# Kernel tuning notes

Hardware: AMD Instinct MI355X
Metric: run time of the kernel (lower is better)

## Reference

```python
import jax, jax.numpy as jnp
import numpy as np


def setup_inputs() -> dict:
    key = jax.random.key(0)
    k1, k2, k3 = jax.random.split(key, 3)
    B, U, D0, D1 = 256, 512, 512, 1024
    x = jax.random.normal(k1, (B, D0), dtype=jnp.float32)
    y = jax.random.normal(k2, (B, D1), dtype=jnp.float32)
    # Glorot-uniform-ish scale for the bilinear weight
    limit = np.sqrt(6.0 / (D0 + D1)).astype(np.float32)
    w = jax.random.uniform(k3, (U, D0, D1), dtype=jnp.float32, minval=-limit, maxval=limit)
    b = jnp.zeros((U,), dtype=jnp.float32)
    return {"x": x, "y": y, "w": w, "b": b}


def reference(x, y, w, b):
    # out[b,u] = sum_{i,j} x[b,i] * w[u,i,j] * y[b,j] + b[u]
    # Two chained GEMMs instead of materializing (B,U,D0,D1):
    xw = jnp.einsum('bi,uij->buj', x, w)   # (B, U, D1)
    out = jnp.einsum('buj,bj->bu', xw, y) + b  # (B, U)
    return out
```

## Files before the change

### kernel.cpp

```cpp
#include <hip/hip_runtime.h>
#include <hip/hip_bf16.h>

typedef float f32x4 __attribute__((ext_vector_type(4)));
typedef short s16x8 __attribute__((ext_vector_type(8)));

#define NB   256
#define NU   512
#define ND0  512
#define ND1  1024
#define WROW (ND0 * ND1)

__device__ __forceinline__ unsigned int f2bf_pk(float a, float b) {
  __hip_bfloat16 ha = __float2bfloat16(a);
  __hip_bfloat16 hb = __float2bfloat16(b);
  unsigned short ua, ub;
  __builtin_memcpy(&ua, &ha, 2);
  __builtin_memcpy(&ub, &hb, 2);
  return (unsigned int)ua | ((unsigned int)ub << 16);
}

__device__ __forceinline__ void block_sync_lds() {
  asm volatile("s_waitcnt lgkmcnt(0)" ::: "memory");
  __builtin_amdgcn_s_barrier();
}

__global__ __launch_bounds__(256) void init_out(const float* __restrict__ bias,
                                                float* __restrict__ out) {
  int idx = blockIdx.x * 256 + threadIdx.x;
  out[idx] = bias[idx & (NU - 1)];
}

__global__ __launch_bounds__(512, 4) void bilinear_kern(
    const float* __restrict__ x, const float* __restrict__ y,
    const float* __restrict__ w, float* __restrict__ out) {
  __shared__ char Alds[32768];
  __shared__ char Wlds[16384];

  const int t    = threadIdx.x;
  const int lane = t & 63;
  const int l15  = lane & 15;
  const int lk   = lane >> 4;
  const int wid  = t >> 6;
  const int wm   = wid >> 2;
  const int wn   = wid & 3;

  const int nt    = blockIdx.x & 3;
  const int ic    = blockIdx.x >> 2;
  const int ucol0 = nt * 128 + wn * 32;

  f32x4 acc[8][2];
#pragma unroll
  for (int mf = 0; mf < 8; ++mf)
#pragma unroll
    for (int nf = 0; nf < 2; ++nf)
#pragma unroll
      for (int r = 0; r < 4; ++r) acc[mf][nf][r] = 0.0f;

  const int ar   = t >> 4;
  const int aswz = (ar & 7) << 4;
  const int awr  = ar * 128 + ((l15 * 8) ^ aswz);
  const float* yb = y + (size_t)ar * ND1 + l15 * 4;

  const int wrb = wid * 16 + lk;
  const float* wq = w + (size_t)(nt * 128 + wrb) * WROW + l15 * 4;

  const int afswz = (l15 & 7) << 4;

  f32x4 wv[4], wvn[4];
  {
    const float* p0 = wq + (size_t)(ic * 4) * ND1;
#pragma unroll
    for (int q = 0; q < 4; ++q)
      wv[q] = __builtin_nontemporal_load((const f32x4*)(p0 + (size_t)q * 4 * WROW));
  }
  float xv[8];
#pragma unroll
  for (int p = 0; p < 8; ++p)
    xv[p] = x[(size_t)(ar + 32 * p) * ND0 + ic * 4];

  for (int it = 0; it < 64; ++it) {
    const int j0 = (it & 15) * 64;

    block_sync_lds();

#pragma unroll
    for (int g = 0; g < 2; ++g) {
      f32x4 v[4];
#pragma unroll
      for (int pp = 0; pp < 4; ++pp)
        v[pp] = *(const f32x4*)(yb + (size_t)(g * 4 + pp) * 32 * ND1 + j0);
#pragma unroll
      for (int pp = 0; pp < 4; ++pp) {
        const int p = g * 4 + pp;
        unsigned long long pk =
            (unsigned long long)f2bf_pk(xv[p] * v[pp][0], xv[p] * v[pp][1]) |
            ((unsigned long long)f2bf_pk(xv[p] * v[pp][2], xv[p] * v[pp][3]) << 32);
        *(unsigned long long*)(Alds + awr + p * 4096) = pk;
      }
    }

#pragma unroll
    for (int q = 0; q < 4; ++q) {
      const int row  = wrb + 4 * q;
      const int byte = row * 128 + ((l15 * 8) ^ ((row & 7) << 4));
      unsigned long long pk =
          (unsigned long long)f2bf_pk(wv[q][0], wv[q][1]) |
          ((unsigned long long)f2bf_pk(wv[q][2], wv[q][3]) << 32);
      *(unsigned long long*)(Wlds + byte) = pk;
    }

    if (it < 63) {
      const int tn = it + 1;
      const int ii = ic * 4 + (tn >> 4);
      const int jn = (tn & 15) * 64;
      const float* pn = wq + (size_t)ii * ND1 + jn;
#pragma unroll
      for (int q = 0; q < 4; ++q)
        wvn[q] = __builtin_nontemporal_load((const f32x4*)(pn + (size_t)q * 4 * WROW));
      if ((it & 15) == 15) {
#pragma unroll
        for (int pp = 0; pp < 8; ++pp)
          xv[pp] = x[(size_t)(ar + 32 * pp) * ND0 + ii];
      }
    }

    block_sync_lds();

#pragma unroll
    for (int ks = 0; ks < 2; ++ks) {
      const int kcol = ks * 64;
      s16x8 bf[2];
#pragma unroll
      for (int nf = 0; nf < 2; ++nf) {
        const int row = wn * 32 + nf * 16 + l15;
        bf[nf] = *(const s16x8*)(Wlds + row * 128 + ((kcol + lk * 16) ^ afswz));
      }
#pragma unroll
      for (int mf = 0; mf < 8; ++mf) {
        const int row = wm * 128 + mf * 16 + l15;
        s16x8 af = *(const s16x8*)(Alds + row * 128 + ((kcol + lk * 16) ^ afswz));
        acc[mf][0] = __builtin_amdgcn_mfma_f32_16x16x32_bf16(af, bf[0], acc[mf][0], 0, 0, 0);
        acc[mf][1] = __builtin_amdgcn_mfma_f32_16x16x32_bf16(af, bf[1], acc[mf][1], 0, 0, 0);
      }
    }

#pragma unroll
    for (int q = 0; q < 4; ++q) wv[q] = wvn[q];
  }

#pragma unroll
  for (int mf = 0; mf < 8; ++mf) {
    const int grow = wm * 128 + mf * 16 + lk * 4;
#pragma unroll
    for (int nf = 0; nf < 2; ++nf) {
      const int gcol = ucol0 + nf * 16 + l15;
#pragma unroll
      for (int r = 0; r < 4; ++r) {
        atomicAdd(out + (size_t)(grow + r) * NU + gcol, acc[mf][nf][r]);
      }
    }
  }
}

extern "C" void kernel_launch(void* const* d_in, const int* in_sizes, int n_in,
                              void* d_out, int out_size, void* d_ws, size_t ws_size,
                              hipStream_t stream) {
  const float* x    = (const float*)d_in[0];
  const float* y    = (const float*)d_in[1];
  const float* w    = (const float*)d_in[2];
  const float* bias = (const float*)d_in[3];
  float* out = (float*)d_out;

  init_out<<<512, 256, 0, stream>>>(bias, out);
  bilinear_kern<<<512, 512, 0, stream>>>(x, y, w, out);
}
```

Before: 297.6 us.

## Stream W via global_load_lds double buffer with 1024-thread blocks

Loads fp32 weight tiles straight into LDS with global_load_lds, double-buffered and swizzled, so weights no longer pass through registers. Conversion to bf16 now happens when the MFMA operands are read back from LDS. Blocks grow to 1024 threads and the grid halves, so each block covers 8 i-values instead of 4 and the atomic output traffic drops. The cost is twice the LDS footprint per block and repeated bf16 conversion of W fragments by every wave that reads them.

```diff
diff --git a/kernel.cpp b/kernel.cpp
--- a/kernel.cpp
+++ b/kernel.cpp
@@ -24,17 +24,23 @@
   __builtin_amdgcn_s_barrier();
 }
 
+__device__ __forceinline__ void glds16(const void* g, void* l) {
+  __builtin_amdgcn_global_load_lds(
+      (const __attribute__((address_space(1))) void*)g,
+      (__attribute__((address_space(3))) void*)l, 16, 0, 0);
+}
+
 __global__ __launch_bounds__(256) void init_out(const float* __restrict__ bias,
                                                 float* __restrict__ out) {
   int idx = blockIdx.x * 256 + threadIdx.x;
   out[idx] = bias[idx & (NU - 1)];
 }
 
-__global__ __launch_bounds__(512, 4) void bilinear_kern(
+__global__ __launch_bounds__(1024, 4) void bilinear_kern(
     const float* __restrict__ x, const float* __restrict__ y,
     const float* __restrict__ w, float* __restrict__ out) {
-  __shared__ char Alds[32768];
-  __shared__ char Wlds[16384];
+  __shared__ __align__(16) char Alds[32768];
+  __shared__ __align__(16) char Wlds[65536];
 
   const int t    = threadIdx.x;
   const int lane = t & 63;
@@ -48,109 +54,98 @@
   const int ic    = blockIdx.x >> 2;
   const int ucol0 = nt * 128 + wn * 32;
 
-  f32x4 acc[8][2];
+  f32x4 acc[4][2];
 #pragma unroll
-  for (int mf = 0; mf < 8; ++mf)
+  for (int mf = 0; mf < 4; ++mf)
 #pragma unroll
     for (int nf = 0; nf < 2; ++nf)
 #pragma unroll
       for (int r = 0; r < 4; ++r) acc[mf][nf][r] = 0.0f;
 
   const int ar   = t >> 4;
-  const int aswz = (ar & 7) << 4;
-  const int awr  = ar * 128 + ((l15 * 8) ^ aswz);
+  const int awr  = ar * 128 + ((l15 * 8) ^ ((ar & 7) << 4));
   const float* yb = y + (size_t)ar * ND1 + l15 * 4;
 
-  const int wrb = wid * 16 + lk;
-  const float* wq = w + (size_t)(nt * 128 + wrb) * WROW + l15 * 4;
+  const float* wg0 = w + (size_t)(nt * 128 + wid * 8 + lk) * WROW
+                       + ((l15 ^ lk) * 4);
+  const float* wg1 = w + (size_t)(nt * 128 + wid * 8 + 4 + lk) * WROW
+                       + ((l15 ^ (4 + lk)) * 4);
+  char* wd = Wlds + wid * 2048;
 
   const int afswz = (l15 & 7) << 4;
 
-  f32x4 wv[4], wvn[4];
   {
-    const float* p0 = wq + (size_t)(ic * 4) * ND1;
-#pragma unroll
-    for (int q = 0; q < 4; ++q)
-      wv[q] = __builtin_nontemporal_load((const f32x4*)(p0 + (size_t)q * 4 * WROW));
+    const size_t o0 = (size_t)(ic * 8) * ND1;
+    glds16(wg0 + o0, wd);
+    glds16(wg1 + o0, wd + 1024);
   }
-  float xv[8];
-#pragma unroll
-  for (int p = 0; p < 8; ++p)
-    xv[p] = x[(size_t)(ar + 32 * p) * ND0 + ic * 4];
 
-  for (int it = 0; it < 64; ++it) {
+  float xv[4];
+
+  for (int it = 0; it < 128; ++it) {
     const int j0 = (it & 15) * 64;
+    const int ii = ic * 8 + (it >> 4);
 
     block_sync_lds();
 
+    if ((it & 15) == 0) {
 #pragma unroll
-    for (int g = 0; g < 2; ++g) {
-      f32x4 v[4];
-#pragma unroll
-      for (int pp = 0; pp < 4; ++pp)
-        v[pp] = *(const f32x4*)(yb + (size_t)(g * 4 + pp) * 32 * ND1 + j0);
-#pragma unroll
-      for (int pp = 0; pp < 4; ++pp) {
-        const int p = g * 4 + pp;
-        unsigned long long pk =
-            (unsigned long long)f2bf_pk(xv[p] * v[pp][0], xv[p] * v[pp][1]) |
-            ((unsigned long long)f2bf_pk(xv[p] * v[pp][2], xv[p] * v[pp][3]) << 32);
-        *(unsigned long long*)(Alds + awr + p * 4096) = pk;
-      }
+      for (int p = 0; p < 4; ++p)
+        xv[p] = x[(size_t)(ar + 64 * p) * ND0 + ii];
+    }
+
+    if (it < 127) {
+      const int tn  = it + 1;
+      const size_t on = (size_t)(ic * 8 + (tn >> 4)) * ND1 + (size_t)((tn & 15) * 64);
+      char* dst = wd + ((size_t)(tn & 1) << 15);
+      glds16(wg0 + on, dst);
+      glds16(wg1 + on, dst + 1024);
     }
 
 #pragma unroll
-    for (int q = 0; q < 4; ++q) {
-      const int row  = wrb + 4 * q;
-      const int byte = row * 128 + ((l15 * 8) ^ ((row & 7) << 4));
+    for (int p = 0; p < 4; ++p) {
+      f32x4 v = *(const f32x4*)(yb + (size_t)p * 64 * ND1 + j0);
       unsigned long long pk =
-          (unsigned long long)f2bf_pk(wv[q][0], wv[q][1]) |
-          ((unsigned long long)f2bf_pk(wv[q][2], wv[q][3]) << 32);
-      *(unsigned long long*)(Wlds + byte) = pk;
+          (unsigned long long)f2bf_pk(xv[p] * v[0], xv[p] * v[1]) |
+          ((unsigned long long)f2bf_pk(xv[p] * v[2], xv[p] * v[3]) << 32);
+      *(unsigned long long*)(Alds + awr + p * 8192) = pk;
     }
 
-    if (it < 63) {
-      const int tn = it + 1;
-      const int ii = ic * 4 + (tn >> 4);
-      const int jn = (tn & 15) * 64;
-      const float* pn = wq + (size_t)ii * ND1 + jn;
-#pragma unroll
-      for (int q = 0; q < 4; ++q)
-        wvn[q] = __builtin_nontemporal_load((const f32x4*)(pn + (size_t)q * 4 * WROW));
-      if ((it & 15) == 15) {
-#pragma unroll
-        for (int pp = 0; pp < 8; ++pp)
-          xv[pp] = x[(size_t)(ar + 32 * pp) * ND0 + ii];
-      }
-    }
+    if (it < 127)
+      asm volatile("s_waitcnt vmcnt(2) lgkmcnt(0)" ::: "memory");
+    else
+      asm volatile("s_waitcnt vmcnt(0) lgkmcnt(0)" ::: "memory");
+    __builtin_amdgcn_s_barrier();
 
-    block_sync_lds();
-
+    const char* Wcur = Wlds + ((size_t)(it & 1) << 15);
 #pragma unroll
     for (int ks = 0; ks < 2; ++ks) {
-      const int kcol = ks * 64;
-      s16x8 bf[2];
+      s16x8 bfr[2];
 #pragma unroll
       for (int nf = 0; nf < 2; ++nf) {
         const int row = wn * 32 + nf * 16 + l15;
-        bf[nf] = *(const s16x8*)(Wlds + row * 128 + ((kcol + lk * 16) ^ afswz));
+        const int r7  = row & 7;
+        const int c0  = ks * 8 + lk * 2;
+        const char* base = Wcur + row * 256;
+        f32x4 wlo = *(const f32x4*)(base + ((c0 ^ r7) << 4));
+        f32x4 whi = *(const f32x4*)(base + (((c0 + 1) ^ r7) << 4));
+        unsigned int pk[4] = { f2bf_pk(wlo[0], wlo[1]), f2bf_pk(wlo[2], wlo[3]),
+                               f2bf_pk(whi[0], whi[1]), f2bf_pk(whi[2], whi[3]) };
+        __builtin_memcpy(&bfr[nf], pk, 16);
       }
 #pragma unroll
-      for (int mf = 0; mf < 8; ++mf) {
-        const int row = wm * 128 + mf * 16 + l15;
-        s16x8 af = *(const s16x8*)(Alds + row * 128 + ((kcol + lk * 16) ^ afswz));
-        acc[mf][0] = __builtin_amdgcn_mfma_f32_16x16x32_bf16(af, bf[0], acc[mf][0], 0, 0, 0);
-        acc[mf][1] = __builtin_amdgcn_mfma_f32_16x16x32_bf16(af, bf[1], acc[mf][1], 0, 0, 0);
+      for (int mf = 0; mf < 4; ++mf) {
+        const int row = wm * 64 + mf * 16 + l15;
+        s16x8 af = *(const s16x8*)(Alds + row * 128 + ((ks * 64 + lk * 16) ^ afswz));
+        acc[mf][0] = __builtin_amdgcn_mfma_f32_16x16x32_bf16(af, bfr[0], acc[mf][0], 0, 0, 0);
+        acc[mf][1] = __builtin_amdgcn_mfma_f32_16x16x32_bf16(af, bfr[1], acc[mf][1], 0, 0, 0);
       }
     }
-
-#pragma unroll
-    for (int q = 0; q < 4; ++q) wv[q] = wvn[q];
   }
 
 #pragma unroll
-  for (int mf = 0; mf < 8; ++mf) {
-    const int grow = wm * 128 + mf * 16 + lk * 4;
+  for (int mf = 0; mf < 4; ++mf) {
+    const int grow = wm * 64 + mf * 16 + lk * 4;
 #pragma unroll
     for (int nf = 0; nf < 2; ++nf) {
       const int gcol = ucol0 + nf * 16 + l15;
@@ -172,5 +167,5 @@
   float* out = (float*)d_out;
 
   init_out<<<512, 256, 0, stream>>>(bias, out);
-  bilinear_kern<<<512, 512, 0, stream>>>(x, y, w, out);
+  bilinear_kern<<<256, 1024, 0, stream>>>(x, y, w, out);
 }
```

New measurement: 455.0 us. +52.9%, slower.
